# Performance work log

Hardware: AMD Instinct MI355X
Metric: run time of the kernel (lower is better)

## Reference

```python
import jax, jax.numpy as jnp
import numpy as np

N = 100000   # nodes
E = 800000   # edges (before self-loops)
IN = 256     # in_channels
HID = 32     # hidden_channels per head
H = 8        # heads in layer 1
OUT = 40     # num classes
NEG_SLOPE = 0.2  # PyG GATConv default


def gat_conv(x, src, dst, W, att_src, att_dst, bias, concat):
    """PyG-style GATConv (inference). x:[N,F], W:[F,H*C], att_*:[H,C], bias:[H*C or C]."""
    n = x.shape[0]
    heads, ch = att_src.shape
    h = (x @ W).reshape(n, heads, ch)                      # [N,H,C]
    a_src = (h * att_src[None]).sum(-1)                    # [N,H]
    a_dst = (h * att_dst[None]).sum(-1)                    # [N,H]
    logits = a_src[src] + a_dst[dst]                       # [E,H]
    logits = jax.nn.leaky_relu(logits, NEG_SLOPE)
    # segment softmax over destination nodes
    m = jax.ops.segment_max(logits, dst, num_segments=n)   # [N,H]
    m = jnp.where(jnp.isfinite(m), m, 0.0)                 # guard empty segments
    ex = jnp.exp(logits - m[dst])                          # [E,H]
    denom = jax.ops.segment_sum(ex, dst, num_segments=n)   # [N,H]
    alpha = ex / (denom[dst] + 1e-16)                      # [E,H]
    msg = h[src] * alpha[..., None]                        # [E,H,C]
    out = jax.ops.segment_sum(msg, dst, num_segments=n)    # [N,H,C]
    out = out.reshape(n, heads * ch) if concat else out.mean(axis=1)
    return out + bias


def setup_inputs() -> dict:
    key = jax.random.key(0)
    ks = jax.random.split(key, 10)
    x = jax.random.normal(ks[0], (N, IN), jnp.float32)
    edge_index = jax.random.randint(ks[1], (2, E), 0, N, dtype=jnp.int32)
    W1 = jax.random.normal(ks[2], (IN, H * HID), jnp.float32) / np.sqrt(IN)
    att_src1 = jax.random.normal(ks[3], (H, HID), jnp.float32) / np.sqrt(HID)
    att_dst1 = jax.random.normal(ks[4], (H, HID), jnp.float32) / np.sqrt(HID)
    b1 = jnp.zeros((H * HID,), jnp.float32)
    W2 = jax.random.normal(ks[5], (H * HID, OUT), jnp.float32) / np.sqrt(H * HID)
    att_src2 = jax.random.normal(ks[6], (1, OUT), jnp.float32) / np.sqrt(OUT)
    att_dst2 = jax.random.normal(ks[7], (1, OUT), jnp.float32) / np.sqrt(OUT)
    b2 = jnp.zeros((OUT,), jnp.float32)
    return {"x": x, "edge_index": edge_index, "W1": W1, "att_src1": att_src1,
            "att_dst1": att_dst1, "b1": b1, "W2": W2, "att_src2": att_src2,
            "att_dst2": att_dst2, "b2": b2}


def reference(x, edge_index, W1, att_src1, att_dst1, b1, W2, att_src2, att_dst2, b2):
    # add self-loops (PyG GATConv default)
    loops = jnp.arange(N, dtype=edge_index.dtype)
    src = jnp.concatenate([edge_index[0], loops])
    dst = jnp.concatenate([edge_index[1], loops])
    h = gat_conv(x, src, dst, W1, att_src1, att_dst1, b1, concat=True)
    h = jax.nn.elu(h)
    return gat_conv(h, src, dst, W2, att_src2, att_dst2, b2, concat=False)
```

## Files before the change

kernel.cpp:

```cpp
#include <hip/hip_runtime.h>
#include <math.h>

#define NSLOPE 0.2f

__device__ __forceinline__ float lrelu(float x){ return x > 0.f ? x : NSLOPE * x; }
__device__ __forceinline__ float eluf(float x){ return x > 0.f ? x : expm1f(x); }

__device__ __forceinline__ unsigned short f2bf(float f) {
  unsigned u = __float_as_uint(f);
  u = (u + 0x7fff + ((u >> 16) & 1)) >> 16;
  return (unsigned short)u;
}
__device__ __forceinline__ unsigned pk2bf(float a, float b) {
  return (unsigned)f2bf(a) | ((unsigned)f2bf(b) << 16);
}

typedef __attribute__((ext_vector_type(8))) short bf16x8;
typedef __attribute__((ext_vector_type(4))) float f32x4;

__global__ __launch_bounds__(256) void conv_w_kernel(const float* __restrict__ W,
                                                     unsigned short* __restrict__ wt) {
  int n = blockIdx.x;
  int k = threadIdx.x;
  wt[n * 256 + k] = f2bf(W[k * 256 + n]);
}

__global__ __launch_bounds__(256) void gemm1_mfma_kernel(const float* __restrict__ x,
                                                         const unsigned short* __restrict__ wt,
                                                         unsigned short* __restrict__ h1b,
                                                         int N) {
  __shared__ __align__(16) unsigned short Asl[128][40];
  __shared__ __align__(16) unsigned short Bsl[128][40];
  int tid = threadIdx.x;
  int bm = blockIdx.x >> 1, bn = blockIdx.x & 1;
  int row0 = bm * 128, col0 = bn * 128;

  int lr = tid >> 2;
  int lk = (tid & 3) * 8;

  int lane = tid & 63, wv = tid >> 6;
  int m0 = (wv & 1) * 64, n0 = (wv >> 1) * 64;
  int lm = lane & 15, quad = lane >> 4;

  f32x4 acc[4][4];
#pragma unroll
  for (int i = 0; i < 4; ++i)
#pragma unroll
    for (int j = 0; j < 4; ++j) acc[i][j] = (f32x4){0.f, 0.f, 0.f, 0.f};

  for (int kc = 0; kc < 256; kc += 32) {
    float4 a0 = {0,0,0,0}, a1 = {0,0,0,0}, a2 = {0,0,0,0}, a3 = {0,0,0,0};
    int r0 = row0 + lr, r1 = row0 + 64 + lr;
    if (r0 < N) {
      const float4* s0 = (const float4*)(x + (size_t)r0 * 256 + kc + lk);
      a0 = s0[0]; a1 = s0[1];
    }
    if (r1 < N) {
      const float4* s1 = (const float4*)(x + (size_t)r1 * 256 + kc + lk);
      a2 = s1[0]; a3 = s1[1];
    }
    uint4 bv0 = *(const uint4*)(wt + (size_t)(col0 + lr) * 256 + kc + lk);
    uint4 bv1 = *(const uint4*)(wt + (size_t)(col0 + 64 + lr) * 256 + kc + lk);
    uint4 pa0, pa1;
    pa0.x = pk2bf(a0.x, a0.y); pa0.y = pk2bf(a0.z, a0.w);
    pa0.z = pk2bf(a1.x, a1.y); pa0.w = pk2bf(a1.z, a1.w);
    pa1.x = pk2bf(a2.x, a2.y); pa1.y = pk2bf(a2.z, a2.w);
    pa1.z = pk2bf(a3.x, a3.y); pa1.w = pk2bf(a3.z, a3.w);
    __syncthreads();
    *(uint4*)&Asl[lr][lk]      = pa0;
    *(uint4*)&Asl[64 + lr][lk] = pa1;
    *(uint4*)&Bsl[lr][lk]      = bv0;
    *(uint4*)&Bsl[64 + lr][lk] = bv1;
    __syncthreads();
    bf16x8 aF[4], bF[4];
#pragma unroll
    for (int i = 0; i < 4; ++i) aF[i] = *(const bf16x8*)&Asl[m0 + i * 16 + lm][quad * 8];
#pragma unroll
    for (int j = 0; j < 4; ++j) bF[j] = *(const bf16x8*)&Bsl[n0 + j * 16 + lm][quad * 8];
#pragma unroll
    for (int i = 0; i < 4; ++i)
#pragma unroll
      for (int j = 0; j < 4; ++j)
        acc[i][j] = __builtin_amdgcn_mfma_f32_16x16x32_bf16(aF[i], bF[j], acc[i][j], 0, 0, 0);
  }

#pragma unroll
  for (int i = 0; i < 4; ++i) {
#pragma unroll
    for (int j = 0; j < 4; ++j) {
      int gc = col0 + n0 + j * 16 + lm;
      int grb = row0 + m0 + i * 16 + quad * 4;
#pragma unroll
      for (int r = 0; r < 4; ++r) {
        int grow = grb + r;
        if (grow < N) h1b[(size_t)grow * 256 + gc] = f2bf(acc[i][j][r]);
      }
    }
  }
}

__global__ __launch_bounds__(256) void att1_kernel(const unsigned short* __restrict__ h1b,
                                                   const float* __restrict__ att_src,
                                                   const float* __restrict__ att_dst,
                                                   float* __restrict__ a_src,
                                                   float* __restrict__ a_dst, int N) {
  __shared__ float sas[256];
  __shared__ float sad[256];
  int tid = threadIdx.x;
  sas[tid] = att_src[tid];
  sad[tid] = att_dst[tid];
  __syncthreads();
  int gid = blockIdx.x * 256 + tid;
  if (gid >= N * 8) return;
  int h = gid & 7;
  const uint4* hv = (const uint4*)(h1b + (size_t)(gid >> 3) * 256 + h * 32);
  float s1 = 0.f, s2 = 0.f;
#pragma unroll
  for (int q = 0; q < 4; ++q) {
    uint4 u = hv[q];
    unsigned uu[4] = {u.x, u.y, u.z, u.w};
#pragma unroll
    for (int e = 0; e < 4; ++e) {
      float lo = __uint_as_float(uu[e] << 16);
      float hi = __uint_as_float(uu[e] & 0xffff0000u);
      int c = h * 32 + q * 8 + e * 2;
      s1 += lo * sas[c] + hi * sas[c + 1];
      s2 += lo * sad[c] + hi * sad[c + 1];
    }
  }
  a_src[gid] = s1;
  a_dst[gid] = s2;
}

__global__ void count_kernel(const int* __restrict__ ei, int* __restrict__ cnt, int E, int N) {
  int e = blockIdx.x * 256 + threadIdx.x;
  if (e >= E + N) return;
  int d = (e < E) ? ei[E + e] : (e - E);
  atomicAdd(&cnt[d], 1);
}

__global__ __launch_bounds__(256) void scan1_kernel(const int* __restrict__ cnt,
                                                    int* __restrict__ tmp,
                                                    int* __restrict__ bsum, int N) {
  __shared__ int sh[256];
  int t = threadIdx.x;
  int base = blockIdx.x * 1024 + t * 4;
  int v[4]; int s = 0;
#pragma unroll
  for (int j = 0; j < 4; ++j) { v[j] = (base + j < N) ? cnt[base + j] : 0; s += v[j]; }
  sh[t] = s;
  __syncthreads();
  for (int off = 1; off < 256; off <<= 1) {
    int xv = (t >= off) ? sh[t - off] : 0;
    __syncthreads();
    sh[t] += xv;
    __syncthreads();
  }
  if (t == 255) bsum[blockIdx.x] = sh[255];
  int run = sh[t] - s;
#pragma unroll
  for (int j = 0; j < 4; ++j) {
    if (base + j < N) tmp[base + j] = run;
    run += v[j];
  }
}

__global__ __launch_bounds__(128) void scan2_kernel(const int* __restrict__ bsum,
                                                    int* __restrict__ boff, int nb) {
  __shared__ int sh[128];
  int t = threadIdx.x;
  int v = (t < nb) ? bsum[t] : 0;
  sh[t] = v;
  __syncthreads();
  for (int off = 1; off < 128; off <<= 1) {
    int xv = (t >= off) ? sh[t - off] : 0;
    __syncthreads();
    sh[t] += xv;
    __syncthreads();
  }
  if (t < nb) boff[t] = sh[t] - v;
}

__global__ void scan3_kernel(const int* __restrict__ tmp, const int* __restrict__ boff,
                             int* __restrict__ row_ptr, int* __restrict__ cursor,
                             int N, int Etot) {
  int i = blockIdx.x * 256 + threadIdx.x;
  if (i == 0) row_ptr[N] = Etot;
  if (i >= N) return;
  int rp = tmp[i] + boff[i >> 10];
  row_ptr[i] = rp;
  cursor[i] = rp;
}

__global__ void fill_kernel(const int* __restrict__ ei, int* __restrict__ cursor,
                            int* __restrict__ col, int E, int N) {
  int e = blockIdx.x * 256 + threadIdx.x;
  if (e >= E + N) return;
  int s, d;
  if (e < E) { s = ei[e]; d = ei[E + e]; } else { s = e - E; d = s; }
  int pos = atomicAdd(&cursor[d], 1);
  col[pos] = s;
}

__global__ __launch_bounds__(256) void agg1_kernel(const unsigned short* __restrict__ h1b,
                                                   const float* __restrict__ a_src,
                                                   const float* __restrict__ a_dst,
                                                   const int* __restrict__ row_ptr,
                                                   const int* __restrict__ col,
                                                   const float* __restrict__ b1,
                                                   unsigned short* __restrict__ hmidb, int N) {
  int lane = threadIdx.x & 63;
  int n = blockIdx.x * 4 + (threadIdx.x >> 6);
  if (n >= N) return;
  int beg = row_ptr[n], deg = row_ptr[n + 1] - beg;

  int hA = lane & 7, eoA = lane >> 3;
  float adst = a_dst[n * 8 + hA];

  int half = lane >> 5;
  int cl = lane & 31;
  int hB = cl >> 2;
  float4 acc0 = {0.f,0.f,0.f,0.f}, acc1 = {0.f,0.f,0.f,0.f};
  float den = 0.f;

  for (int c0 = 0; c0 < deg; c0 += 8) {
    int eb = c0 + eoA;
    int ec = eb < deg ? eb : deg - 1;
    int sB = col[beg + ec];
    float exB = 0.f;
    if (eb < deg) exB = __expf(lrelu(a_src[sB * 8 + hA] + adst));
    den += exB;
    int rem = deg - c0; if (rem > 8) rem = 8;
#pragma unroll
    for (int p = 0; p < 4; ++p) {
      int myE = 2 * p + half;
      int s = __shfl(sB, myE * 8);
      float al = __shfl(exB, myE * 8 + hB);
      if (myE < rem) {
        uint4 hv = *(const uint4*)(h1b + (size_t)s * 256 + cl * 8);
        acc0.x = fmaf(al, __uint_as_float(hv.x << 16), acc0.x);
        acc0.y = fmaf(al, __uint_as_float(hv.x & 0xffff0000u), acc0.y);
        acc0.z = fmaf(al, __uint_as_float(hv.y << 16), acc0.z);
        acc0.w = fmaf(al, __uint_as_float(hv.y & 0xffff0000u), acc0.w);
        acc1.x = fmaf(al, __uint_as_float(hv.z << 16), acc1.x);
        acc1.y = fmaf(al, __uint_as_float(hv.z & 0xffff0000u), acc1.y);
        acc1.z = fmaf(al, __uint_as_float(hv.w << 16), acc1.z);
        acc1.w = fmaf(al, __uint_as_float(hv.w & 0xffff0000u), acc1.w);
      }
    }
  }
#pragma unroll
  for (int off = 8; off < 64; off <<= 1) den += __shfl_xor(den, off);
  float invden = 1.f / (den + 1e-16f);
  float invB = __shfl(invden, hB);

  float po[8] = {acc0.x, acc0.y, acc0.z, acc0.w, acc1.x, acc1.y, acc1.z, acc1.w};
#pragma unroll
  for (int j = 0; j < 8; ++j) po[j] += __shfl(po[j], cl + 32);
  if (half == 0) {
    const float4* b4 = (const float4*)(b1 + cl * 8);
    float4 bb0 = b4[0], bb1 = b4[1];
    float r0 = eluf(fmaf(po[0], invB, bb0.x)), r1 = eluf(fmaf(po[1], invB, bb0.y));
    float r2 = eluf(fmaf(po[2], invB, bb0.z)), r3 = eluf(fmaf(po[3], invB, bb0.w));
    float r4 = eluf(fmaf(po[4], invB, bb1.x)), r5 = eluf(fmaf(po[5], invB, bb1.y));
    float r6 = eluf(fmaf(po[6], invB, bb1.z)), r7 = eluf(fmaf(po[7], invB, bb1.w));
    uint4 ov;
    ov.x = pk2bf(r0, r1); ov.y = pk2bf(r2, r3);
    ov.z = pk2bf(r4, r5); ov.w = pk2bf(r6, r7);
    *(uint4*)(hmidb + (size_t)n * 256 + cl * 8) = ov;
  }
}

__global__ __launch_bounds__(256) void gemm2_mfma_kernel(const unsigned short* __restrict__ hmidb,
                                                         const float* __restrict__ W2,
                                                         const float* __restrict__ as2,
                                                         const float* __restrict__ ad2,
                                                         unsigned short* __restrict__ h2b,
                                                         float* __restrict__ a_src2,
                                                         float* __restrict__ a_dst2, int N) {
  __shared__ __align__(16) unsigned short Asl[128][40];
  __shared__ __align__(16) unsigned short Bs[48][264];
  __shared__ float asv[48], adv[48];
  int tid = threadIdx.x;
  for (int i = tid; i < 48 * 264 / 2; i += 256) ((unsigned*)Bs)[i] = 0;
  if (tid < 48) {
    asv[tid] = (tid < 40) ? as2[tid] : 0.f;
    adv[tid] = (tid < 40) ? ad2[tid] : 0.f;
  }
  __syncthreads();
  for (int i = tid; i < 256 * 40; i += 256) {
    int k = i / 40, c = i - k * 40;
    Bs[c][k] = f2bf(W2[i]);
  }

  int row0 = blockIdx.x * 128;
  int lane = tid & 63, wv = tid >> 6;
  int lm = lane & 15, quad = lane >> 4;
  int lr = tid >> 1;
  int lk = (tid & 1) * 16;

  f32x4 acc[2][3];
#pragma unroll
  for (int i = 0; i < 2; ++i)
#pragma unroll
    for (int j = 0; j < 3; ++j) acc[i][j] = (f32x4){0.f,0.f,0.f,0.f};

  for (int kc = 0; kc < 256; kc += 32) {
    uint4 v0 = {0,0,0,0}, v1 = {0,0,0,0};
    int r = row0 + lr;
    if (r < N) {
      const uint4* src = (const uint4*)(hmidb + (size_t)r * 256 + kc + lk);
      v0 = src[0]; v1 = src[1];
    }
    __syncthreads();
    *(uint4*)&Asl[lr][lk]     = v0;
    *(uint4*)&Asl[lr][lk + 8] = v1;
    __syncthreads();
    bf16x8 aF[2], bF[3];
#pragma unroll
    for (int i = 0; i < 2; ++i) aF[i] = *(const bf16x8*)&Asl[wv * 32 + i * 16 + lm][quad * 8];
#pragma unroll
    for (int j = 0; j < 3; ++j) bF[j] = *(const bf16x8*)&Bs[j * 16 + lm][kc + quad * 8];
#pragma unroll
    for (int i = 0; i < 2; ++i)
#pragma unroll
      for (int j = 0; j < 3; ++j)
        acc[i][j] = __builtin_amdgcn_mfma_f32_16x16x32_bf16(aF[i], bF[j], acc[i][j], 0, 0, 0);
  }

#pragma unroll
  for (int i = 0; i < 2; ++i) {
#pragma unroll
    for (int r = 0; r < 4; ++r) {
      int grow = row0 + wv * 32 + i * 16 + quad * 4 + r;
      float vs = 0.f, vd = 0.f;
#pragma unroll
      for (int j = 0; j < 3; ++j) {
        vs = fmaf(acc[i][j][r], asv[j * 16 + lm], vs);
        vd = fmaf(acc[i][j][r], adv[j * 16 + lm], vd);
      }
#pragma unroll
      for (int off = 1; off < 16; off <<= 1) {
        vs += __shfl_xor(vs, off);
        vd += __shfl_xor(vd, off);
      }
      if (grow < N) {
#pragma unroll
        for (int j = 0; j < 3; ++j) {
          int c = j * 16 + lm;
          if (c < 40) h2b[(size_t)grow * 40 + c] = f2bf(acc[i][j][r]);
        }
        if (lm == 0) { a_src2[grow] = vs; a_dst2[grow] = vd; }
      }
    }
  }
}

__global__ __launch_bounds__(256) void agg2_kernel(const unsigned short* __restrict__ h2b,
                                                   const float* __restrict__ a_src,
                                                   const float* __restrict__ a_dst,
                                                   const int* __restrict__ row_ptr,
                                                   const int* __restrict__ col,
                                                   const float* __restrict__ b2,
                                                   float* __restrict__ out, int N) {
  int lane = threadIdx.x & 63;
  int n = blockIdx.x * 4 + (threadIdx.x >> 6);
  if (n >= N) return;
  int beg = row_ptr[n], deg = row_ptr[n + 1] - beg;
  float adst = a_dst[n];

  int eg = lane / 10;
  int cg = lane % 10;
  bool active = lane < 60;
  float4 acc = {0.f,0.f,0.f,0.f};
  float den = 0.f;

  for (int c0 = 0; c0 < deg; c0 += 60) {
    int eb = c0 + lane;
    int ec = eb < deg ? eb : deg - 1;
    int sB = col[beg + ec];
    float ex = 0.f;
    if (lane < 60 && eb < deg) ex = __expf(lrelu(a_src[sB] + adst));
    den += ex;
    int rem = deg - c0; if (rem > 60) rem = 60;
    int nst = (rem + 5) / 6;
    for (int st = 0; st < nst; ++st) {
      int lsrc = st * 6 + eg;
      float al = __shfl(ex, lsrc);
      int s = __shfl(sB, lsrc);
      if (active && (c0 + lsrc) < deg) {
        uint2 hv = *(const uint2*)(h2b + (size_t)s * 40 + cg * 4);
        acc.x = fmaf(al, __uint_as_float(hv.x << 16), acc.x);
        acc.y = fmaf(al, __uint_as_float(hv.x & 0xffff0000u), acc.y);
        acc.z = fmaf(al, __uint_as_float(hv.y << 16), acc.z);
        acc.w = fmaf(al, __uint_as_float(hv.y & 0xffff0000u), acc.w);
      }
    }
  }
#pragma unroll
  for (int off = 1; off < 64; off <<= 1) den += __shfl_xor(den, off);
  float inv = 1.f / (den + 1e-16f);

  float4 o = acc;
#pragma unroll
  for (int k = 1; k < 6; ++k) {
    int src = lane + 10 * k;
    o.x += __shfl(acc.x, src);
    o.y += __shfl(acc.y, src);
    o.z += __shfl(acc.z, src);
    o.w += __shfl(acc.w, src);
  }
  if (lane < 10) {
    float4 bb = *(const float4*)(b2 + cg * 4);
    o.x = fmaf(o.x, inv, bb.x);
    o.y = fmaf(o.y, inv, bb.y);
    o.z = fmaf(o.z, inv, bb.z);
    o.w = fmaf(o.w, inv, bb.w);
    *(float4*)(out + (size_t)n * 40 + cg * 4) = o;
  }
}

extern "C" void kernel_launch(void* const* d_in, const int* in_sizes, int n_in,
                              void* d_out, int out_size, void* d_ws, size_t ws_size,
                              hipStream_t stream) {
  const float* x   = (const float*)d_in[0];
  const int*   ei  = (const int*)d_in[1];
  const float* W1  = (const float*)d_in[2];
  const float* as1 = (const float*)d_in[3];
  const float* ad1 = (const float*)d_in[4];
  const float* b1  = (const float*)d_in[5];
  const float* W2  = (const float*)d_in[6];
  const float* as2 = (const float*)d_in[7];
  const float* ad2 = (const float*)d_in[8];
  const float* b2  = (const float*)d_in[9];
  float* out = (float*)d_out;

  int N = in_sizes[0] / 256;
  int E = in_sizes[1] / 2;
  int Etot = E + N;

  char* p = (char*)d_ws;
  auto alloc = [&](size_t bytes) -> char* {
    char* r = p;
    p += (bytes + 255) & ~(size_t)255;
    return r;
  };
  unsigned short* w1t   = (unsigned short*)alloc((size_t)256 * 256 * 2);
  unsigned short* h1b   = (unsigned short*)alloc((size_t)N * 256 * 2);
  unsigned short* hmidb = (unsigned short*)alloc((size_t)N * 256 * 2);
  unsigned short* h2b   = (unsigned short*)alloc((size_t)N * 40 * 2);
  float* a_src1 = (float*)alloc((size_t)N * 8 * 4);
  float* a_dst1 = (float*)alloc((size_t)N * 8 * 4);
  float* a_src2 = (float*)alloc((size_t)N * 4);
  float* a_dst2 = (float*)alloc((size_t)N * 4);
  int* cnt      = (int*)alloc((size_t)N * 4);
  int* cursor   = (int*)alloc((size_t)N * 4);
  int* row_ptr  = (int*)alloc(((size_t)N + 1) * 4);
  int* tmp      = (int*)alloc((size_t)N * 4);
  int* bsum     = (int*)alloc(512);
  int* boff     = (int*)alloc(512);
  int* colx     = (int*)alloc((size_t)Etot * 4);

  hipMemsetAsync(cnt, 0, (size_t)N * 4, stream);

  int nbE = (Etot + 255) / 256;
  int nb1 = (N + 1023) / 1024;
  count_kernel<<<nbE, 256, 0, stream>>>(ei, cnt, E, N);
  scan1_kernel<<<nb1, 256, 0, stream>>>(cnt, tmp, bsum, N);
  scan2_kernel<<<1, 128, 0, stream>>>(bsum, boff, nb1);
  scan3_kernel<<<(N + 255) / 256, 256, 0, stream>>>(tmp, boff, row_ptr, cursor, N, Etot);
  fill_kernel<<<nbE, 256, 0, stream>>>(ei, cursor, colx, E, N);

  conv_w_kernel<<<256, 256, 0, stream>>>(W1, w1t);
  gemm1_mfma_kernel<<<((N + 127) / 128) * 2, 256, 0, stream>>>(x, w1t, h1b, N);
  att1_kernel<<<(N * 8 + 255) / 256, 256, 0, stream>>>(h1b, as1, ad1, a_src1, a_dst1, N);
  agg1_kernel<<<(N + 3) / 4, 256, 0, stream>>>(h1b, a_src1, a_dst1, row_ptr, colx, b1, hmidb, N);
  gemm2_mfma_kernel<<<(N + 127) / 128, 256, 0, stream>>>(hmidb, W2, as2, ad2, h2b, a_src2, a_dst2, N);
  agg2_kernel<<<(N + 3) / 4, 256, 0, stream>>>(h2b, a_src2, a_dst2, row_ptr, colx, b2, out, N);
}
```

Before: 450.8 us.

## Fuse layer-1 attention coefficients into GEMM epilogue and trim aggregation loop

Computes a_src/a_dst for layer 1 in the MFMA GEMM epilogue from fp32 accumulators, using 16-lane shuffle reductions, and drops the separate att1 kernel that re-read h1b. The agg1 inner loop now runs only for valid edge pairs instead of a fixed unroll of four. Gather offsets use 32-bit unsigned arithmetic, and ELU uses __expf(x)-1 instead of expm1f. The epilogue adds shuffle work and register pressure to the GEMM, and the attention logits now come from fp32 rather than bf16-rounded values, which slightly changes the numerics.

```diff
diff --git a/kernel.cpp b/kernel.cpp
--- a/kernel.cpp
+++ b/kernel.cpp
@@ -4,7 +4,7 @@
 #define NSLOPE 0.2f
 
 __device__ __forceinline__ float lrelu(float x){ return x > 0.f ? x : NSLOPE * x; }
-__device__ __forceinline__ float eluf(float x){ return x > 0.f ? x : expm1f(x); }
+__device__ __forceinline__ float eluf(float x){ return x > 0.f ? x : __expf(x) - 1.f; }
 
 __device__ __forceinline__ unsigned short f2bf(float f) {
   unsigned u = __float_as_uint(f);
@@ -27,7 +27,11 @@
 
 __global__ __launch_bounds__(256) void gemm1_mfma_kernel(const float* __restrict__ x,
                                                          const unsigned short* __restrict__ wt,
+                                                         const float* __restrict__ att_src,
+                                                         const float* __restrict__ att_dst,
                                                          unsigned short* __restrict__ h1b,
+                                                         float* __restrict__ a_src,
+                                                         float* __restrict__ a_dst,
                                                          int N) {
   __shared__ __align__(16) unsigned short Asl[128][40];
   __shared__ __align__(16) unsigned short Bsl[128][40];
@@ -84,6 +88,15 @@
         acc[i][j] = __builtin_amdgcn_mfma_f32_16x16x32_bf16(aF[i], bF[j], acc[i][j], 0, 0, 0);
   }
 
+  float avs[4], avd[4];
+#pragma unroll
+  for (int j = 0; j < 4; ++j) {
+    int gc = col0 + n0 + j * 16 + lm;
+    avs[j] = att_src[gc];
+    avd[j] = att_dst[gc];
+  }
+  int headA = (col0 + n0) >> 5;
+
 #pragma unroll
   for (int i = 0; i < 4; ++i) {
 #pragma unroll
@@ -96,40 +109,28 @@
         if (grow < N) h1b[(size_t)grow * 256 + gc] = f2bf(acc[i][j][r]);
       }
     }
-  }
-}
-
-__global__ __launch_bounds__(256) void att1_kernel(const unsigned short* __restrict__ h1b,
-                                                   const float* __restrict__ att_src,
-                                                   const float* __restrict__ att_dst,
-                                                   float* __restrict__ a_src,
-                                                   float* __restrict__ a_dst, int N) {
-  __shared__ float sas[256];
-  __shared__ float sad[256];
-  int tid = threadIdx.x;
-  sas[tid] = att_src[tid];
-  sad[tid] = att_dst[tid];
-  __syncthreads();
-  int gid = blockIdx.x * 256 + tid;
-  if (gid >= N * 8) return;
-  int h = gid & 7;
-  const uint4* hv = (const uint4*)(h1b + (size_t)(gid >> 3) * 256 + h * 32);
-  float s1 = 0.f, s2 = 0.f;
-#pragma unroll
-  for (int q = 0; q < 4; ++q) {
-    uint4 u = hv[q];
-    unsigned uu[4] = {u.x, u.y, u.z, u.w};
-#pragma unroll
-    for (int e = 0; e < 4; ++e) {
-      float lo = __uint_as_float(uu[e] << 16);
-      float hi = __uint_as_float(uu[e] & 0xffff0000u);
-      int c = h * 32 + q * 8 + e * 2;
-      s1 += lo * sas[c] + hi * sas[c + 1];
-      s2 += lo * sad[c] + hi * sad[c + 1];
-    }
-  }
-  a_src[gid] = s1;
-  a_dst[gid] = s2;
+#pragma unroll
+    for (int r = 0; r < 4; ++r) {
+      int grow = row0 + m0 + i * 16 + quad * 4 + r;
+      float sA = acc[i][0][r] * avs[0] + acc[i][1][r] * avs[1];
+      float dA = acc[i][0][r] * avd[0] + acc[i][1][r] * avd[1];
+      float sB = acc[i][2][r] * avs[2] + acc[i][3][r] * avs[3];
+      float dB = acc[i][2][r] * avd[2] + acc[i][3][r] * avd[3];
+#pragma unroll
+      for (int off = 1; off < 16; off <<= 1) {
+        sA += __shfl_xor(sA, off);
+        dA += __shfl_xor(dA, off);
+        sB += __shfl_xor(sB, off);
+        dB += __shfl_xor(dB, off);
+      }
+      if (lm == 0 && grow < N) {
+        a_src[grow * 8 + headA]     = sA;
+        a_dst[grow * 8 + headA]     = dA;
+        a_src[grow * 8 + headA + 1] = sB;
+        a_dst[grow * 8 + headA + 1] = dB;
+      }
+    }
+  }
 }
 
 __global__ void count_kernel(const int* __restrict__ ei, int* __restrict__ cnt, int E, int N) {
@@ -215,7 +216,7 @@
   int beg = row_ptr[n], deg = row_ptr[n + 1] - beg;
 
   int hA = lane & 7, eoA = lane >> 3;
-  float adst = a_dst[n * 8 + hA];
+  float adst = a_dst[(unsigned)n * 8u + hA];
 
   int half = lane >> 5;
   int cl = lane & 31;
@@ -224,20 +225,21 @@
   float den = 0.f;
 
   for (int c0 = 0; c0 < deg; c0 += 8) {
+    int rem = deg - c0; if (rem > 8) rem = 8;
     int eb = c0 + eoA;
     int ec = eb < deg ? eb : deg - 1;
     int sB = col[beg + ec];
     float exB = 0.f;
-    if (eb < deg) exB = __expf(lrelu(a_src[sB * 8 + hA] + adst));
+    if (eoA < rem) exB = __expf(lrelu(a_src[(unsigned)sB * 8u + hA] + adst));
     den += exB;
-    int rem = deg - c0; if (rem > 8) rem = 8;
-#pragma unroll
-    for (int p = 0; p < 4; ++p) {
+    int pmax = (rem + 1) >> 1;
+    for (int p = 0; p < pmax; ++p) {
       int myE = 2 * p + half;
       int s = __shfl(sB, myE * 8);
       float al = __shfl(exB, myE * 8 + hB);
       if (myE < rem) {
-        uint4 hv = *(const uint4*)(h1b + (size_t)s * 256 + cl * 8);
+        unsigned off = (unsigned)s * 256u + (unsigned)(cl * 8);
+        uint4 hv = *(const uint4*)(h1b + off);
         acc0.x = fmaf(al, __uint_as_float(hv.x << 16), acc0.x);
         acc0.y = fmaf(al, __uint_as_float(hv.x & 0xffff0000u), acc0.y);
         acc0.z = fmaf(al, __uint_as_float(hv.y << 16), acc0.z);
@@ -389,7 +391,8 @@
       float al = __shfl(ex, lsrc);
       int s = __shfl(sB, lsrc);
       if (active && (c0 + lsrc) < deg) {
-        uint2 hv = *(const uint2*)(h2b + (size_t)s * 40 + cg * 4);
+        unsigned off = (unsigned)s * 40u + (unsigned)(cg * 4);
+        uint2 hv = *(const uint2*)(h2b + off);
         acc.x = fmaf(al, __uint_as_float(hv.x << 16), acc.x);
         acc.y = fmaf(al, __uint_as_float(hv.x & 0xffff0000u), acc.y);
         acc.z = fmaf(al, __uint_as_float(hv.y << 16), acc.z);
@@ -472,8 +475,7 @@
   fill_kernel<<<nbE, 256, 0, stream>>>(ei, cursor, colx, E, N);
 
   conv_w_kernel<<<256, 256, 0, stream>>>(W1, w1t);
-  gemm1_mfma_kernel<<<((N + 127) / 128) * 2, 256, 0, stream>>>(x, w1t, h1b, N);
-  att1_kernel<<<(N * 8 + 255) / 256, 256, 0, stream>>>(h1b, as1, ad1, a_src1, a_dst1, N);
+  gemm1_mfma_kernel<<<((N + 127) / 128) * 2, 256, 0, stream>>>(x, w1t, as1, ad1, h1b, a_src1, a_dst1, N);
   agg1_kernel<<<(N + 3) / 4, 256, 0, stream>>>(h1b, a_src1, a_dst1, row_ptr, colx, b1, hmidb, N);
   gemm2_mfma_kernel<<<(N + 127) / 128, 256, 0, stream>>>(hmidb, W2, as2, ad2, h2b, a_src2, a_dst2, N);
   agg2_kernel<<<(N + 3) / 4, 256, 0, stream>>>(h2b, a_src2, a_dst2, row_ptr, colx, b2, out, N);
```

After: 465.2 us. +3.2%, slower.
